# Kernel optimization log

Measured on AMD Instinct MI355X. Metric: run time of the kernel, lower is better.

Reference implementation:

```python
import jax, jax.numpy as jnp
import numpy as np
import math

N = 100000      # active voxels
K = 27          # 3**3 kernel offsets
L = 50000
INC = 64
OUTC = 64


def setup_inputs() -> dict:
    key = jax.random.key(0)
    k1, k2, k3, k4 = jax.random.split(key, 4)
    features = jax.random.normal(k1, (N, INC), dtype=jnp.float32)
    # kernel init: uniform(-std, std), std = 1/sqrt(inc * k^3)
    std = 1.0 / math.sqrt(INC * K)
    kernel = jax.random.uniform(k2, (K, INC, OUTC), dtype=jnp.float32,
                                minval=-std, maxval=std)
    neighbor_in = jax.random.randint(k3, (K, L), 0, N, dtype=jnp.int32)
    neighbor_out = jax.random.randint(k4, (K, L), 0, N, dtype=jnp.int32)
    return {"features": features, "kernel": kernel,
            "neighbor_in": neighbor_in, "neighbor_out": neighbor_out}


def reference(features, kernel, neighbor_in, neighbor_out):
    # gather -> per-offset GEMM -> scatter-add (torchsparse sparseconv_op, transpose=False)
    gathered = features[neighbor_in]                      # [K, L, INC]
    vals = jnp.einsum('klc,kco->klo', gathered, kernel)    # [K, L, OUTC]
    out = jnp.zeros((features.shape[0], kernel.shape[-1]), dtype=features.dtype)
    out = out.at[neighbor_out.reshape(-1)].add(vals.reshape(-1, kernel.shape[-1]))
    return out
```

## Files before the change

kernel.cpp:

```cpp
#include <hip/hip_runtime.h>
#include <hip/hip_bf16.h>


typedef __bf16 bf16x8 __attribute__((ext_vector_type(8)));
typedef float f32x4 __attribute__((ext_vector_type(4)));

#define KOFF 27
#define SLOTK 4
#define NSLOT (KOFF * SLOTK)
#define OVFCAP 8192
#define WPAD 72
#define ROWCHUNK 8192
#define NIBW (ROWCHUNK / 8)

__global__ __launch_bounds__(256) void kA_rank_cast(
    const float* __restrict__ feat, const float* __restrict__ kern,
    const int* __restrict__ nout, __bf16* __restrict__ fb,
    __bf16* __restrict__ wt, unsigned short* __restrict__ slots,
    int2* __restrict__ ovf, int* __restrict__ ovfcnt, int Lpairs, int nElems,
    int nchunk, int rankBlocks, int wtBlocks) {
  __shared__ unsigned int nib[NIBW];
  if ((int)blockIdx.x < rankBlocks) {
    const int k = blockIdx.x / nchunk;
    const int chunk = blockIdx.x % nchunk;
    const int lo = chunk * ROWCHUNK;
    const int tid = threadIdx.x;
    for (int i = tid; i < NIBW; i += 256) nib[i] = 0u;
    __syncthreads();
    const int* nk = nout + k * Lpairs;
    for (int base = 0; base < Lpairs; base += 2048) {
      int l[8], row[8];
#pragma unroll
      for (int j = 0; j < 8; ++j) {
        l[j] = base + j * 256 + tid;
        row[j] = (l[j] < Lpairs) ? nk[l[j]] : -1;
      }
#pragma unroll
      for (int j = 0; j < 8; ++j) {
        int rr = row[j] - lo;
        if (rr >= 0 && rr < ROWCHUNK) {
          unsigned int sh = ((unsigned)rr & 7u) * 4u;
          unsigned int old = atomicAdd(&nib[rr >> 3], 1u << sh);
          int rank = (old >> sh) & 15;
          if (rank < SLOTK) {
            slots[(size_t)row[j] * NSLOT + k * SLOTK + rank] =
                (unsigned short)l[j];
          } else {
            int idx = atomicAdd(ovfcnt, 1);
            if (idx < OVFCAP) ovf[idx] = make_int2(row[j], k * Lpairs + l[j]);
          }
        }
      }
    }
  } else if ((int)blockIdx.x < rankBlocks + wtBlocks) {
    int kc = (blockIdx.x - rankBlocks) * 256 + threadIdx.x;
    if (kc < KOFF * 64) {
      int k = kc >> 6, c = kc & 63;
      const float* src = kern + k * 4096 + c;
      __bf16* dst = wt + (size_t)kc * 64;
#pragma unroll
      for (int i0 = 0; i0 < 64; i0 += 8) {
        bf16x8 v;
#pragma unroll
        for (int q = 0; q < 8; ++q) v[q] = (__bf16)src[(i0 + q) * 64];
        *(bf16x8*)(dst + i0) = v;
      }
    }
  } else {
    int i = ((blockIdx.x - rankBlocks - wtBlocks) * 256 + threadIdx.x) * 8;
    if (i < nElems) {
      f32x4 a = *(const f32x4*)(feat + i);
      f32x4 b = *(const f32x4*)(feat + i + 4);
      bf16x8 v;
#pragma unroll
      for (int j = 0; j < 4; ++j) {
        v[j] = (__bf16)a[j];
        v[j + 4] = (__bf16)b[j];
      }
      *(bf16x8*)(fb + i) = v;
    }
  }
}

__global__ __launch_bounds__(256) void kF_fused(
    const __bf16* __restrict__ fb, const __bf16* __restrict__ wt,
    const int* __restrict__ nin, const unsigned short* __restrict__ slots,
    float* __restrict__ out, int Lpairs, int Nrows) {
  __shared__ __bf16 ldsW[2][64 * WPAD];
  const int tid = threadIdx.x;
  const int wv = tid >> 6, lane = tid & 63;
  const int r = lane & 15, g = lane >> 4;
  int row = blockIdx.x * 64 + wv * 16 + r;
  if (row >= Nrows) row = Nrows - 1;
  const unsigned short* srow = slots + (size_t)row * NSLOT;

  const int sc = tid >> 2;
  const int si = (tid & 3) * 16;

  {
    const __bf16* wp = wt + sc * 64 + si;
    bf16x8 wa = *(const bf16x8*)(wp);
    bf16x8 wb = *(const bf16x8*)(wp + 8);
    *(bf16x8*)&ldsW[0][sc * WPAD + si] = wa;
    *(bf16x8*)&ldsW[0][sc * WPAD + si + 8] = wb;
  }

  uint2 sv0 = *(const uint2*)(srow);
  uint2 sv1 = *(const uint2*)(srow + SLOTK);
  int e[4] = {(int)(sv0.x & 0xFFFF), (int)(sv0.x >> 16),
              (int)(sv0.y & 0xFFFF), (int)(sv0.y >> 16)};
  int en[4] = {(int)(sv1.x & 0xFFFF), (int)(sv1.x >> 16),
               (int)(sv1.y & 0xFFFF), (int)(sv1.y >> 16)};
  int irow[4], irown[4];
#pragma unroll
  for (int j = 0; j < 4; ++j) irow[j] = (e[j] != 0xFFFF) ? nin[e[j]] : -1;

  f32x4 acc[4] = {f32x4{0.f, 0.f, 0.f, 0.f}, f32x4{0.f, 0.f, 0.f, 0.f},
                  f32x4{0.f, 0.f, 0.f, 0.f}, f32x4{0.f, 0.f, 0.f, 0.f}};
  __syncthreads();

  for (int k = 0; k < KOFF; ++k) {
    const int kb = k & 1;
    bf16x8 fa[4], fc[4];
#pragma unroll
    for (int j = 0; j < 4; ++j) {
      if (irow[j] >= 0) {
        const __bf16* ap = fb + (size_t)irow[j] * 64 + g * 8;
        fa[j] = *(const bf16x8*)(ap);
        fc[j] = *(const bf16x8*)(ap + 32);
      }
    }
    const int* ninK1 = nin + (k + 1) * Lpairs;
#pragma unroll
    for (int j = 0; j < 4; ++j)
      irown[j] = (k + 1 < KOFF && en[j] != 0xFFFF) ? ninK1[en[j]] : -1;
    uint2 sv2 = make_uint2(0xFFFFFFFFu, 0xFFFFFFFFu);
    if (k + 2 < KOFF) sv2 = *(const uint2*)(srow + (k + 2) * SLOTK);
    if (k + 1 < KOFF) {
      const __bf16* wp = wt + (size_t)(k + 1) * 4096 + sc * 64 + si;
      bf16x8 wa = *(const bf16x8*)(wp);
      bf16x8 wb = *(const bf16x8*)(wp + 8);
      *(bf16x8*)&ldsW[kb ^ 1][sc * WPAD + si] = wa;
      *(bf16x8*)&ldsW[kb ^ 1][sc * WPAD + si + 8] = wb;
    }
    float s0[8] = {0.f, 0.f, 0.f, 0.f, 0.f, 0.f, 0.f, 0.f};
    float s1[8] = {0.f, 0.f, 0.f, 0.f, 0.f, 0.f, 0.f, 0.f};
#pragma unroll
    for (int j = 0; j < 4; ++j) {
      if (irow[j] >= 0) {
#pragma unroll
        for (int q = 0; q < 8; ++q) {
          s0[q] += (float)fa[j][q];
          s1[q] += (float)fc[j][q];
        }
      }
    }
    bf16x8 b0, b1;
#pragma unroll
    for (int q = 0; q < 8; ++q) {
      b0[q] = (__bf16)s0[q];
      b1[q] = (__bf16)s1[q];
    }
    bf16x8 w0f[4], w1f[4];
#pragma unroll
    for (int t = 0; t < 4; ++t) {
      w0f[t] = *(const bf16x8*)&ldsW[kb][(t * 16 + r) * WPAD + g * 8];
      w1f[t] = *(const bf16x8*)&ldsW[kb][(t * 16 + r) * WPAD + g * 8 + 32];
    }
#pragma unroll
    for (int t = 0; t < 4; ++t) {
      acc[t] = __builtin_amdgcn_mfma_f32_16x16x32_bf16(w0f[t], b0, acc[t], 0, 0, 0);
      acc[t] = __builtin_amdgcn_mfma_f32_16x16x32_bf16(w1f[t], b1, acc[t], 0, 0, 0);
    }
    __syncthreads();
#pragma unroll
    for (int j = 0; j < 4; ++j) irow[j] = irown[j];
    en[0] = (int)(sv2.x & 0xFFFF);
    en[1] = (int)(sv2.x >> 16);
    en[2] = (int)(sv2.y & 0xFFFF);
    en[3] = (int)(sv2.y >> 16);
  }

  float* op = out + (size_t)row * 64;
#pragma unroll
  for (int t = 0; t < 4; ++t) *(f32x4*)(op + t * 16 + g * 4) = acc[t];
}

__global__ __launch_bounds__(256) void k4_fixup(
    const __bf16* __restrict__ fb, const __bf16* __restrict__ wt,
    const int* __restrict__ nin, const int2* __restrict__ ovf,
    const int* __restrict__ ovfcnt, float* __restrict__ out, int Lpairs) {
  int gid = blockIdx.x * 256 + threadIdx.x;
  int i = gid >> 6, c = gid & 63;
  int n = *ovfcnt;
  if (n > OVFCAP) n = OVFCAP;
  if (i >= n) return;
  int row = ovf[i].x, pid = ovf[i].y;
  int k = pid / Lpairs;
  int irow = nin[pid];
  const __bf16* wk = wt + ((size_t)k * 64 + c) * 64;
  const __bf16* f = fb + (size_t)irow * 64;
  float s = 0.f;
#pragma unroll 8
  for (int q = 0; q < 64; ++q) s += (float)f[q] * (float)wk[q];
  atomicAdd(&out[(size_t)row * 64 + c], s);
}

__global__ __launch_bounds__(256) void spconv_atomic_kernel(
    const float* __restrict__ feat, const float* __restrict__ kern,
    const int* __restrict__ nin, const int* __restrict__ nout,
    float* __restrict__ out, int Lpairs, int blocksPerK) {
  __shared__ __bf16 ldsBT[64 * WPAD];
  const int bk = blockIdx.x / blocksPerK;
  const int chunk = blockIdx.x % blocksPerK;
  const float* kb = kern + bk * 4096;
  for (int idx = threadIdx.x; idx < 4096; idx += 256) {
    int i = idx >> 6, c = idx & 63;
    ldsBT[c * WPAD + i] = (__bf16)kb[idx];
  }
  __syncthreads();
  const int lane = threadIdx.x & 63;
  const int wave = threadIdx.x >> 6;
  const int r = lane & 15, g = lane >> 4;
  bf16x8 bfrag[2][4];
#pragma unroll
  for (int s = 0; s < 2; ++s)
#pragma unroll
    for (int t = 0; t < 4; ++t)
      bfrag[s][t] = *(const bf16x8*)&ldsBT[(t * 16 + r) * WPAD + g * 8 + s * 32];
  const int* ninK = nin + bk * Lpairs;
  const int* noutK = nout + bk * Lpairs;
  const int base0 = chunk * 512 + wave * 128;
  for (int it = 0; it < 8; ++it) {
    const int base = base0 + it * 16;
    if (base >= Lpairs) break;
    const int arow = ninK[base + r];
    const float* ap = feat + (size_t)arow * 64 + g * 8;
    f32x4 f0 = *(const f32x4*)(ap);
    f32x4 f1 = *(const f32x4*)(ap + 4);
    f32x4 f2 = *(const f32x4*)(ap + 32);
    f32x4 f3 = *(const f32x4*)(ap + 36);
    bf16x8 a0, a1;
#pragma unroll
    for (int j = 0; j < 4; ++j) {
      a0[j] = (__bf16)f0[j];
      a0[j + 4] = (__bf16)f1[j];
      a1[j] = (__bf16)f2[j];
      a1[j + 4] = (__bf16)f3[j];
    }
    f32x4 acc[4] = {f32x4{0.f, 0.f, 0.f, 0.f}, f32x4{0.f, 0.f, 0.f, 0.f},
                    f32x4{0.f, 0.f, 0.f, 0.f}, f32x4{0.f, 0.f, 0.f, 0.f}};
#pragma unroll
    for (int t = 0; t < 4; ++t) {
      acc[t] = __builtin_amdgcn_mfma_f32_16x16x32_bf16(a0, bfrag[0][t], acc[t], 0, 0, 0);
      acc[t] = __builtin_amdgcn_mfma_f32_16x16x32_bf16(a1, bfrag[1][t], acc[t], 0, 0, 0);
    }
    int orow[4];
#pragma unroll
    for (int reg = 0; reg < 4; ++reg) orow[reg] = noutK[base + g * 4 + reg];
#pragma unroll
    for (int t = 0; t < 4; ++t)
#pragma unroll
      for (int reg = 0; reg < 4; ++reg)
        atomicAdd(out + (size_t)orow[reg] * 64 + t * 16 + r, acc[t][reg]);
  }
}

extern "C" void kernel_launch(void* const* d_in, const int* in_sizes, int n_in,
                              void* d_out, int out_size, void* d_ws, size_t ws_size,
                              hipStream_t stream) {
  const float* feat = (const float*)d_in[0];
  const float* kern = (const float*)d_in[1];
  const int* nin = (const int*)d_in[2];
  const int* nout = (const int*)d_in[3];
  float* out = (float*)d_out;

  const int total = in_sizes[2];
  const int Lpairs = total / KOFF;
  const int Nrows = out_size / 64;
  const int nElems = Nrows * 64;

  const size_t slotsBytes = (size_t)Nrows * NSLOT * 2;
  const size_t ovfOff = (slotsBytes + 255) & ~(size_t)255;
  const size_t cntOff = (ovfOff + (size_t)OVFCAP * 8 + 255) & ~(size_t)255;
  const size_t wtOff = (cntOff + 256 + 255) & ~(size_t)255;
  const size_t fbOff = (wtOff + (size_t)KOFF * 4096 * 2 + 255) & ~(size_t)255;
  const size_t needed = fbOff + (size_t)nElems * 2;

  const bool shapeOK = (Lpairs <= 65535) && (Lpairs % 16 == 0) &&
                       (total % KOFF == 0) && (out_size % 64 == 0);

  if (shapeOK && ws_size >= needed) {
    unsigned short* slots = (unsigned short*)d_ws;
    int2* ovf = (int2*)((char*)d_ws + ovfOff);
    int* ovfcnt = (int*)((char*)d_ws + cntOff);
    __bf16* wt = (__bf16*)((char*)d_ws + wtOff);
    __bf16* fb = (__bf16*)((char*)d_ws + fbOff);

    hipMemsetAsync(slots, 0xFF, slotsBytes, stream);
    hipMemsetAsync(ovfcnt, 0, 4, stream);

    const int nchunk = (Nrows + ROWCHUNK - 1) / ROWCHUNK;
    const int rankBlocks = KOFF * nchunk;
    const int wtBlocks = (KOFF * 64 + 255) / 256;
    const int castBlocks = (nElems / 8 + 255) / 256;
    kA_rank_cast<<<rankBlocks + wtBlocks + castBlocks, 256, 0, stream>>>(
        feat, kern, nout, fb, wt, slots, ovf, ovfcnt, Lpairs, nElems, nchunk,
        rankBlocks, wtBlocks);
    kF_fused<<<(Nrows + 63) / 64, 256, 0, stream>>>(fb, wt, nin, slots, out,
                                                    Lpairs, Nrows);
    k4_fixup<<<OVFCAP * 64 / 256, 256, 0, stream>>>(fb, wt, nin, ovf, ovfcnt,
                                                    out, Lpairs);
  } else {
    const int blocksPerK = (Lpairs + 511) / 512;
    hipMemsetAsync(d_out, 0, (size_t)out_size * sizeof(float), stream);
    spconv_atomic_kernel<<<KOFF * blocksPerK, 256, 0, stream>>>(
        feat, kern, nin, nout, out, Lpairs, blocksPerK);
  }
}
```

Baseline: 135.4 us.

## Store resolved input row indices in slot table to drop indirect nin lookup

The ranking pass now reads neighbor_in alongside neighbor_out and writes the input row index (32-bit) straight into the per-output slot table, replacing the 16-bit pair index. The fused gather-GEMM kernel can then load a uint4 of input rows per offset and fetch features directly, removing one dependent global load per neighbor from its pipeline. The weight LDS store and barrier are moved after the MFMAs and skipped on the last offset. In exchange, the slot table doubles in size, so the memset and the slot reads and writes move more bytes, and kA now also reads neighbor_in.

```diff
diff --git a/kernel.cpp b/kernel.cpp
--- a/kernel.cpp
+++ b/kernel.cpp
@@ -15,10 +15,11 @@
 
 __global__ __launch_bounds__(256) void kA_rank_cast(
     const float* __restrict__ feat, const float* __restrict__ kern,
-    const int* __restrict__ nout, __bf16* __restrict__ fb,
-    __bf16* __restrict__ wt, unsigned short* __restrict__ slots,
-    int2* __restrict__ ovf, int* __restrict__ ovfcnt, int Lpairs, int nElems,
-    int nchunk, int rankBlocks, int wtBlocks) {
+    const int* __restrict__ nin, const int* __restrict__ nout,
+    __bf16* __restrict__ fb, __bf16* __restrict__ wt,
+    unsigned int* __restrict__ slots, int2* __restrict__ ovf,
+    int* __restrict__ ovfcnt, int Lpairs, int nElems, int nchunk,
+    int rankBlocks, int wtBlocks) {
   __shared__ unsigned int nib[NIBW];
   if ((int)blockIdx.x < rankBlocks) {
     const int k = blockIdx.x / nchunk;
@@ -27,13 +28,15 @@
     const int tid = threadIdx.x;
     for (int i = tid; i < NIBW; i += 256) nib[i] = 0u;
     __syncthreads();
-    const int* nk = nout + k * Lpairs;
+    const int* nkO = nout + k * Lpairs;
+    const int* nkI = nin + k * Lpairs;
     for (int base = 0; base < Lpairs; base += 2048) {
-      int l[8], row[8];
+      int l[8], row[8], rin[8];
 #pragma unroll
       for (int j = 0; j < 8; ++j) {
         l[j] = base + j * 256 + tid;
-        row[j] = (l[j] < Lpairs) ? nk[l[j]] : -1;
+        row[j] = (l[j] < Lpairs) ? nkO[l[j]] : -1;
+        rin[j] = (l[j] < Lpairs) ? nkI[l[j]] : 0;
       }
 #pragma unroll
       for (int j = 0; j < 8; ++j) {
@@ -44,7 +47,7 @@
           int rank = (old >> sh) & 15;
           if (rank < SLOTK) {
             slots[(size_t)row[j] * NSLOT + k * SLOTK + rank] =
-                (unsigned short)l[j];
+                (unsigned int)rin[j];
           } else {
             int idx = atomicAdd(ovfcnt, 1);
             if (idx < OVFCAP) ovf[idx] = make_int2(row[j], k * Lpairs + l[j]);
@@ -84,15 +87,15 @@
 
 __global__ __launch_bounds__(256) void kF_fused(
     const __bf16* __restrict__ fb, const __bf16* __restrict__ wt,
-    const int* __restrict__ nin, const unsigned short* __restrict__ slots,
-    float* __restrict__ out, int Lpairs, int Nrows) {
+    const unsigned int* __restrict__ slots, float* __restrict__ out,
+    int Nrows) {
   __shared__ __bf16 ldsW[2][64 * WPAD];
   const int tid = threadIdx.x;
   const int wv = tid >> 6, lane = tid & 63;
   const int r = lane & 15, g = lane >> 4;
   int row = blockIdx.x * 64 + wv * 16 + r;
   if (row >= Nrows) row = Nrows - 1;
-  const unsigned short* srow = slots + (size_t)row * NSLOT;
+  const uint4* srow = (const uint4*)(slots + (size_t)row * NSLOT);
 
   const int sc = tid >> 2;
   const int si = (tid & 3) * 16;
@@ -105,15 +108,8 @@
     *(bf16x8*)&ldsW[0][sc * WPAD + si + 8] = wb;
   }
 
-  uint2 sv0 = *(const uint2*)(srow);
-  uint2 sv1 = *(const uint2*)(srow + SLOTK);
-  int e[4] = {(int)(sv0.x & 0xFFFF), (int)(sv0.x >> 16),
-              (int)(sv0.y & 0xFFFF), (int)(sv0.y >> 16)};
-  int en[4] = {(int)(sv1.x & 0xFFFF), (int)(sv1.x >> 16),
-               (int)(sv1.y & 0xFFFF), (int)(sv1.y >> 16)};
-  int irow[4], irown[4];
-#pragma unroll
-  for (int j = 0; j < 4; ++j) irow[j] = (e[j] != 0xFFFF) ? nin[e[j]] : -1;
+  uint4 cellCur = srow[0];
+  uint4 cellNxt = srow[1];
 
   f32x4 acc[4] = {f32x4{0.f, 0.f, 0.f, 0.f}, f32x4{0.f, 0.f, 0.f, 0.f},
                   f32x4{0.f, 0.f, 0.f, 0.f}, f32x4{0.f, 0.f, 0.f, 0.f}};
@@ -121,33 +117,30 @@
 
   for (int k = 0; k < KOFF; ++k) {
     const int kb = k & 1;
+    int gC[4] = {(int)cellCur.x, (int)cellCur.y, (int)cellCur.z,
+                 (int)cellCur.w};
     bf16x8 fa[4], fc[4];
 #pragma unroll
     for (int j = 0; j < 4; ++j) {
-      if (irow[j] >= 0) {
-        const __bf16* ap = fb + (size_t)irow[j] * 64 + g * 8;
+      if (gC[j] >= 0) {
+        const __bf16* ap = fb + (size_t)gC[j] * 64 + g * 8;
         fa[j] = *(const bf16x8*)(ap);
         fc[j] = *(const bf16x8*)(ap + 32);
       }
     }
-    const int* ninK1 = nin + (k + 1) * Lpairs;
-#pragma unroll
-    for (int j = 0; j < 4; ++j)
-      irown[j] = (k + 1 < KOFF && en[j] != 0xFFFF) ? ninK1[en[j]] : -1;
-    uint2 sv2 = make_uint2(0xFFFFFFFFu, 0xFFFFFFFFu);
-    if (k + 2 < KOFF) sv2 = *(const uint2*)(srow + (k + 2) * SLOTK);
+    bf16x8 wa, wb;
     if (k + 1 < KOFF) {
       const __bf16* wp = wt + (size_t)(k + 1) * 4096 + sc * 64 + si;
-      bf16x8 wa = *(const bf16x8*)(wp);
-      bf16x8 wb = *(const bf16x8*)(wp + 8);
-      *(bf16x8*)&ldsW[kb ^ 1][sc * WPAD + si] = wa;
-      *(bf16x8*)&ldsW[kb ^ 1][sc * WPAD + si + 8] = wb;
-    }
+      wa = *(const bf16x8*)(wp);
+      wb = *(const bf16x8*)(wp + 8);
+    }
+    uint4 cv2 = make_uint4(~0u, ~0u, ~0u, ~0u);
+    if (k + 2 < KOFF) cv2 = srow[k + 2];
     float s0[8] = {0.f, 0.f, 0.f, 0.f, 0.f, 0.f, 0.f, 0.f};
     float s1[8] = {0.f, 0.f, 0.f, 0.f, 0.f, 0.f, 0.f, 0.f};
 #pragma unroll
     for (int j = 0; j < 4; ++j) {
-      if (irow[j] >= 0) {
+      if (gC[j] >= 0) {
 #pragma unroll
         for (int q = 0; q < 8; ++q) {
           s0[q] += (float)fa[j][q];
@@ -172,13 +165,13 @@
       acc[t] = __builtin_amdgcn_mfma_f32_16x16x32_bf16(w0f[t], b0, acc[t], 0, 0, 0);
       acc[t] = __builtin_amdgcn_mfma_f32_16x16x32_bf16(w1f[t], b1, acc[t], 0, 0, 0);
     }
-    __syncthreads();
-#pragma unroll
-    for (int j = 0; j < 4; ++j) irow[j] = irown[j];
-    en[0] = (int)(sv2.x & 0xFFFF);
-    en[1] = (int)(sv2.x >> 16);
-    en[2] = (int)(sv2.y & 0xFFFF);
-    en[3] = (int)(sv2.y >> 16);
+    if (k + 1 < KOFF) {
+      *(bf16x8*)&ldsW[kb ^ 1][sc * WPAD + si] = wa;
+      *(bf16x8*)&ldsW[kb ^ 1][sc * WPAD + si + 8] = wb;
+      __syncthreads();
+    }
+    cellCur = cellNxt;
+    cellNxt = cv2;
   }
 
   float* op = out + (size_t)row * 64;
@@ -280,18 +273,18 @@
   const int Nrows = out_size / 64;
   const int nElems = Nrows * 64;
 
-  const size_t slotsBytes = (size_t)Nrows * NSLOT * 2;
+  const size_t slotsBytes = (size_t)Nrows * NSLOT * 4;
   const size_t ovfOff = (slotsBytes + 255) & ~(size_t)255;
   const size_t cntOff = (ovfOff + (size_t)OVFCAP * 8 + 255) & ~(size_t)255;
   const size_t wtOff = (cntOff + 256 + 255) & ~(size_t)255;
   const size_t fbOff = (wtOff + (size_t)KOFF * 4096 * 2 + 255) & ~(size_t)255;
   const size_t needed = fbOff + (size_t)nElems * 2;
 
-  const bool shapeOK = (Lpairs <= 65535) && (Lpairs % 16 == 0) &&
-                       (total % KOFF == 0) && (out_size % 64 == 0);
+  const bool shapeOK = (Lpairs % 16 == 0) && (total % KOFF == 0) &&
+                       (out_size % 64 == 0);
 
   if (shapeOK && ws_size >= needed) {
-    unsigned short* slots = (unsigned short*)d_ws;
+    unsigned int* slots = (unsigned int*)d_ws;
     int2* ovf = (int2*)((char*)d_ws + ovfOff);
     int* ovfcnt = (int*)((char*)d_ws + cntOff);
     __bf16* wt = (__bf16*)((char*)d_ws + wtOff);
@@ -305,10 +298,9 @@
     const int wtBlocks = (KOFF * 64 + 255) / 256;
     const int castBlocks = (nElems / 8 + 255) / 256;
     kA_rank_cast<<<rankBlocks + wtBlocks + castBlocks, 256, 0, stream>>>(
-        feat, kern, nout, fb, wt, slots, ovf, ovfcnt, Lpairs, nElems, nchunk,
-        rankBlocks, wtBlocks);
-    kF_fused<<<(Nrows + 63) / 64, 256, 0, stream>>>(fb, wt, nin, slots, out,
-                                                    Lpairs, Nrows);
+        feat, kern, nin, nout, fb, wt, slots, ovf, ovfcnt, Lpairs, nElems,
+        nchunk, rankBlocks, wtBlocks);
+    kF_fused<<<(Nrows + 63) / 64, 256, 0, stream>>>(fb, wt, slots, out, Nrows);
     k4_fixup<<<OVFCAP * 64 / 256, 256, 0, stream>>>(fb, wt, nin, ovf, ovfcnt,
                                                     out, Lpairs);
   } else {
```

New measurement: 132.4 us. 2.2% less time.
